# Kernel optimization log

Hardware: AMD Instinct MI355X
Metric: run time of the kernel (lower is better)

The kernel has to match this reference:

```python
import jax, jax.numpy as jnp
import numpy as np

N = 4096
D_IN = 512
D_OUT = 512

def setup_inputs() -> dict:
    key = jax.random.key(0)
    k1, k2, k3 = jax.random.split(key, 3)
    X = jax.random.normal(k1, (N, D_IN), dtype=jnp.float32)
    A = jax.random.uniform(k2, (N, N), dtype=jnp.float32)
    # Linear(input_dim, output_dim, bias=False): W is [out, in], y = x @ W.T
    W = jax.random.normal(k3, (D_OUT, D_IN), dtype=jnp.float32) * (1.0 / np.sqrt(D_IN))
    return {"X": X, "A": A, "W": W}

def reference(X, A, W):
    # A2 = A + I
    A2 = A + jnp.eye(A.shape[0], dtype=A.dtype)
    # Dhat = diag(diagonal(A2)); fractional_matrix_power(Dhat, -1/2) on a
    # diagonal matrix is elementwise d^{-1/2}; dense diag GEMMs reduce to
    # row/column scaling.
    dscale = jnp.diagonal(A2) ** (-0.5)  # [N]
    temp = (A2 @ X) @ W.T                # [N, D_OUT]
    A_norm = dscale[:, None] * A2 * dscale[None, :]  # D^-1/2 A2 D^-1/2
    return jax.nn.relu(A_norm @ temp)
```

## Files before the change

### kernel.cpp

```cpp
#include <hip/hip_runtime.h>
#include <hip/hip_bf16.h>
#include <stdint.h>

typedef float  f32x4  __attribute__((ext_vector_type(4)));
typedef __bf16 bf16x8 __attribute__((ext_vector_type(8)));
typedef unsigned short us4 __attribute__((ext_vector_type(4)));

#define NDIM 4096
#define DDIM 512
#define PSTRIDE 2097152

__device__ __forceinline__ unsigned short f2bf(float f) {
    union { float f; uint32_t u; } v; v.f = f;
    uint32_t u = v.u;
    u += 0x7FFFu + ((u >> 16) & 1u);
    return (unsigned short)(u >> 16);
}

__global__ void prep_kernel(const float* __restrict__ A, const float* __restrict__ X,
                            const float* __restrict__ W,
                            unsigned short* __restrict__ A2, unsigned short* __restrict__ Xb,
                            unsigned short* __restrict__ Wb, float* __restrict__ ds) {
    const int b = blockIdx.x, tid = threadIdx.x;
    if (b < 16384) {
        int i = b * 256 + tid;
        int e = i << 2;
        int row = e >> 12, col = e & 4095;
        f32x4 v = ((const f32x4*)A)[i];
        int d = row - col;
        if (d >= 0 && d < 4) v[d] += 1.0f;
        us4 o; o.x = f2bf(v.x); o.y = f2bf(v.y); o.z = f2bf(v.z); o.w = f2bf(v.w);
        ((us4*)A2)[i] = o;
    } else if (b < 18432) {
        int i = (b - 16384) * 256 + tid;
        f32x4 v = ((const f32x4*)X)[i];
        us4 o; o.x = f2bf(v.x); o.y = f2bf(v.y); o.z = f2bf(v.z); o.w = f2bf(v.w);
        ((us4*)Xb)[i] = o;
    } else if (b < 18688) {
        int i = (b - 18432) * 256 + tid;
        f32x4 v = ((const f32x4*)W)[i];
        us4 o; o.x = f2bf(v.x); o.y = f2bf(v.y); o.z = f2bf(v.z); o.w = f2bf(v.w);
        ((us4*)Wb)[i] = o;
    } else {
        int i = (b - 18688) * 256 + tid;
        if (i < NDIM) ds[i] = rsqrtf(A[(size_t)i * (NDIM + 1)] + 1.0f);
    }
}

template <int MODE, int SWAP>
__global__ __launch_bounds__(256, 4) void gemm_bt(
    const unsigned short* __restrict__ A,
    const unsigned short* __restrict__ B,
    void* __restrict__ C,
    int K, int kc, int ldc)
{
    __shared__ unsigned short lsA[128 * 64];
    __shared__ unsigned short lsB[128 * 64];

    const int tid  = threadIdx.x;
    const int wid  = tid >> 6;
    const int lane = tid & 63;
    const int m0 = (SWAP ? blockIdx.y : blockIdx.x) * 128;
    const int n0 = (SWAP ? blockIdx.x : blockIdx.y) * 128;
    const int kbase = blockIdx.z * kc;
    const int wm = (wid & 1) * 64;
    const int wn = (wid >> 1) * 64;

    const int lrow = lane >> 3;
    const int lcs  = (lane & 7) * 16;

    f32x4 acc[4][4];
    #pragma unroll
    for (int i = 0; i < 4; i++)
        #pragma unroll
        for (int j = 0; j < 4; j++) acc[i][j] = (f32x4)0.0f;

    const char* gA = (const char*)A + ((size_t)(m0 + wid * 32 + lrow) * K) * 2 + lcs;
    const char* gB = (const char*)B + ((size_t)(n0 + wid * 32 + lrow) * K) * 2 + lcs;
    const size_t rowstep = (size_t)8 * K * 2;

    for (int k0 = kbase; k0 < kbase + kc; k0 += 64) {
        const size_t kb = (size_t)k0 * 2;
        #pragma unroll
        for (int i = 0; i < 4; i++) {
            __builtin_amdgcn_global_load_lds(
                (const __attribute__((address_space(1))) void*)(gA + kb + (size_t)i * rowstep),
                (__attribute__((address_space(3))) void*)(&lsA[(wid * 4 + i) * 512]),
                16, 0, 0);
            __builtin_amdgcn_global_load_lds(
                (const __attribute__((address_space(1))) void*)(gB + kb + (size_t)i * rowstep),
                (__attribute__((address_space(3))) void*)(&lsB[(wid * 4 + i) * 512]),
                16, 0, 0);
        }
        __syncthreads();

        #pragma unroll
        for (int ks = 0; ks < 2; ks++) {
            const int kboff = ks * 64 + (lane >> 4) * 16;
            bf16x8 bfrag[4], afrag[4];
            #pragma unroll
            for (int nt = 0; nt < 4; nt++) {
                int r = wn + nt * 16 + (lane & 15);
                bfrag[nt] = *(const bf16x8*)((const char*)lsB + r * 128 + kboff);
            }
            #pragma unroll
            for (int mt = 0; mt < 4; mt++) {
                int r = wm + mt * 16 + (lane & 15);
                afrag[mt] = *(const bf16x8*)((const char*)lsA + r * 128 + kboff);
            }
            #pragma unroll
            for (int mt = 0; mt < 4; mt++)
                #pragma unroll
                for (int nt = 0; nt < 4; nt++)
                    acc[mt][nt] = __builtin_amdgcn_mfma_f32_16x16x32_bf16(
                        afrag[mt], bfrag[nt], acc[mt][nt], 0, 0, 0);
        }
        __syncthreads();
    }

    const int col  = lane & 15;
    const int quad = lane >> 4;
    #pragma unroll
    for (int mt = 0; mt < 4; mt++) {
        const int gm0 = m0 + wm + mt * 16 + quad * 4;
        #pragma unroll
        for (int nt = 0; nt < 4; nt++) {
            const int gn = n0 + wn + nt * 16 + col;
            f32x4 v = acc[mt][nt];
            if (MODE == 0) {
                us4 o;
                o.x = f2bf(v.x); o.y = f2bf(v.y); o.z = f2bf(v.z); o.w = f2bf(v.w);
                *(us4*)((unsigned short*)C + (size_t)gn * ldc + gm0) = o;
            } else {
                float* o = (float*)C + (size_t)blockIdx.z * PSTRIDE + (size_t)gm0 * ldc + gn;
                o[0]               = v.x;
                o[ldc]             = v.y;
                o[2 * (size_t)ldc] = v.z;
                o[3 * (size_t)ldc] = v.w;
            }
        }
    }
}

__global__ void ep2_kernel(const float* __restrict__ P, const float* __restrict__ ds,
                           unsigned short* __restrict__ T2) {
    int t = blockIdx.x * 256 + threadIdx.x;
    int e = t << 2;
    int i = e & 4095;
    f32x4 v = ((const f32x4*)P)[t];
    v += ((const f32x4*)(P + PSTRIDE))[t];
    v += ((const f32x4*)(P + 2 * PSTRIDE))[t];
    v += ((const f32x4*)(P + 3 * PSTRIDE))[t];
    f32x4 d = *(const f32x4*)(ds + i);
    us4 o;
    o.x = f2bf(v.x * d.x); o.y = f2bf(v.y * d.y);
    o.z = f2bf(v.z * d.z); o.w = f2bf(v.w * d.w);
    ((us4*)T2)[t] = o;
}

__global__ void ep3_kernel(const float* __restrict__ Q, const float* __restrict__ ds,
                           float* __restrict__ out) {
    int t = blockIdx.x * 256 + threadIdx.x;
    int e = t << 2;
    int i = e >> 9;
    float s = ds[i];
    f32x4 v = ((const f32x4*)Q)[t];
    v += ((const f32x4*)(Q + PSTRIDE))[t];
    v += ((const f32x4*)(Q + 2 * PSTRIDE))[t];
    v += ((const f32x4*)(Q + 3 * PSTRIDE))[t];
    f32x4 o;
    o.x = fmaxf(v.x * s, 0.0f); o.y = fmaxf(v.y * s, 0.0f);
    o.z = fmaxf(v.z * s, 0.0f); o.w = fmaxf(v.w * s, 0.0f);
    ((f32x4*)out)[t] = o;
}

extern "C" void kernel_launch(void* const* d_in, const int* in_sizes, int n_in,
                              void* d_out, int out_size, void* d_ws, size_t ws_size,
                              hipStream_t stream) {
    const float* X = (const float*)d_in[0];
    const float* A = (const float*)d_in[1];
    const float* W = (const float*)d_in[2];

    char* ws = (char*)d_ws;
    float*          dsc  = (float*)ws;
    unsigned short* A2   = (unsigned short*)(ws + 16384);
    unsigned short* Xb   = (unsigned short*)(ws + 33570816u);
    unsigned short* Wb   = (unsigned short*)(ws + 37765120u);
    unsigned short* Yt   = (unsigned short*)(ws + 38289408u);
    unsigned short* T2   = (unsigned short*)(ws + 42483712u);
    float*          Part = (float*)(ws + 46678016u);

    prep_kernel<<<18704, 256, 0, stream>>>(A, X, W, A2, Xb, Wb, dsc);

    gemm_bt<0, 0><<<dim3(32, 4, 1), 256, 0, stream>>>(Xb, Wb, Yt, 512, 512, 4096);
    gemm_bt<2, 1><<<dim3(32, 4, 4), 256, 0, stream>>>(Yt, A2, Part, 4096, 1024, 4096);
    ep2_kernel<<<2048, 256, 0, stream>>>(Part, dsc, T2);
    gemm_bt<2, 0><<<dim3(32, 4, 4), 256, 0, stream>>>(A2, T2, Part, 4096, 1024, 512);
    ep3_kernel<<<2048, 256, 0, stream>>>(Part, dsc, (float*)d_out);
}
```

Baseline: 191.6 us.

## Load small GEMM operand directly to registers, deepen K tile to 128

```diff
diff --git a/kernel.cpp b/kernel.cpp
--- a/kernel.cpp
+++ b/kernel.cpp
@@ -47,15 +47,20 @@
     }
 }
 
-template <int MODE, int SWAP>
-__global__ __launch_bounds__(256, 4) void gemm_bt(
+template <int MODE, int SWAP, int BK, int DIRA, int DIRB>
+__global__ __launch_bounds__(256, 2) void gemm_bt(
     const unsigned short* __restrict__ A,
     const unsigned short* __restrict__ B,
     void* __restrict__ C,
     int K, int kc, int ldc)
 {
-    __shared__ unsigned short lsA[128 * 64];
-    __shared__ unsigned short lsB[128 * 64];
+    constexpr int LPR = BK / 8;
+    constexpr int RPI = 64 / LPR;
+    constexpr int IPW = 128 / (4 * RPI);
+    constexpr int KS  = BK / 32;
+
+    __shared__ unsigned short lsA[DIRA ? 64 : 128 * BK];
+    __shared__ unsigned short lsB[DIRB ? 64 : 128 * BK];
 
     const int tid  = threadIdx.x;
     const int wid  = tid >> 6;
@@ -65,9 +70,11 @@
     const int kbase = blockIdx.z * kc;
     const int wm = (wid & 1) * 64;
     const int wn = (wid >> 1) * 64;
-
-    const int lrow = lane >> 3;
-    const int lcs  = (lane & 7) * 16;
+    const int quad = lane >> 4;
+    const int c16  = lane & 15;
+
+    const int lrow = lane / LPR;
+    const int lcs  = (lane % LPR) * 16;
 
     f32x4 acc[4][4];
     #pragma unroll
@@ -77,36 +84,70 @@
 
     const char* gA = (const char*)A + ((size_t)(m0 + wid * 32 + lrow) * K) * 2 + lcs;
     const char* gB = (const char*)B + ((size_t)(n0 + wid * 32 + lrow) * K) * 2 + lcs;
-    const size_t rowstep = (size_t)8 * K * 2;
-
-    for (int k0 = kbase; k0 < kbase + kc; k0 += 64) {
+    const size_t rowstep = (size_t)RPI * K * 2;
+
+    const char* aDir[4];
+    const char* bDir[4];
+    #pragma unroll
+    for (int t = 0; t < 4; t++) {
+        if (DIRA) aDir[t] = (const char*)A + ((size_t)(m0 + wm + t * 16 + c16) * K) * 2 + quad * 16;
+        if (DIRB) bDir[t] = (const char*)B + ((size_t)(n0 + wn + t * 16 + c16) * K) * 2 + quad * 16;
+    }
+
+    for (int k0 = kbase; k0 < kbase + kc; k0 += BK) {
         const size_t kb = (size_t)k0 * 2;
+        if (!DIRA) {
+            #pragma unroll
+            for (int i = 0; i < IPW; i++)
+                __builtin_amdgcn_global_load_lds(
+                    (const __attribute__((address_space(1))) void*)(gA + kb + (size_t)i * rowstep),
+                    (__attribute__((address_space(3))) void*)(&lsA[(wid * IPW + i) * 512]),
+                    16, 0, 0);
+        }
+        if (!DIRB) {
+            #pragma unroll
+            for (int i = 0; i < IPW; i++)
+                __builtin_amdgcn_global_load_lds(
+                    (const __attribute__((address_space(1))) void*)(gB + kb + (size_t)i * rowstep),
+                    (__attribute__((address_space(3))) void*)(&lsB[(wid * IPW + i) * 512]),
+                    16, 0, 0);
+        }
+        bf16x8 apre[KS][4], bpre[KS][4];
+        if (DIRA) {
+            #pragma unroll
+            for (int ks = 0; ks < KS; ks++)
+                #pragma unroll
+                for (int mt = 0; mt < 4; mt++)
+                    apre[ks][mt] = *(const bf16x8*)(aDir[mt] + kb + ks * 64);
+        }
+        if (DIRB) {
+            #pragma unroll
+            for (int ks = 0; ks < KS; ks++)
+                #pragma unroll
+                for (int nt = 0; nt < 4; nt++)
+                    bpre[ks][nt] = *(const bf16x8*)(bDir[nt] + kb + ks * 64);
+        }
+        __syncthreads();
+
         #pragma unroll
-        for (int i = 0; i < 4; i++) {
-            __builtin_amdgcn_global_load_lds(
-                (const __attribute__((address_space(1))) void*)(gA + kb + (size_t)i * rowstep),
-                (__attribute__((address_space(3))) void*)(&lsA[(wid * 4 + i) * 512]),
-                16, 0, 0);
-            __builtin_amdgcn_global_load_lds(
-                (const __attribute__((address_space(1))) void*)(gB + kb + (size_t)i * rowstep),
-                (__attribute__((address_space(3))) void*)(&lsB[(wid * 4 + i) * 512]),
-                16, 0, 0);
-        }
-        __syncthreads();
-
-        #pragma unroll
-        for (int ks = 0; ks < 2; ks++) {
-            const int kboff = ks * 64 + (lane >> 4) * 16;
+        for (int ks = 0; ks < KS; ks++) {
+            const int kboff = ks * 64 + quad * 16;
             bf16x8 bfrag[4], afrag[4];
             #pragma unroll
             for (int nt = 0; nt < 4; nt++) {
-                int r = wn + nt * 16 + (lane & 15);
-                bfrag[nt] = *(const bf16x8*)((const char*)lsB + r * 128 + kboff);
+                if (DIRB) bfrag[nt] = bpre[ks][nt];
+                else {
+                    int r = wn + nt * 16 + c16;
+                    bfrag[nt] = *(const bf16x8*)((const char*)lsB + r * (BK * 2) + kboff);
+                }
             }
             #pragma unroll
             for (int mt = 0; mt < 4; mt++) {
-                int r = wm + mt * 16 + (lane & 15);
-                afrag[mt] = *(const bf16x8*)((const char*)lsA + r * 128 + kboff);
+                if (DIRA) afrag[mt] = apre[ks][mt];
+                else {
+                    int r = wm + mt * 16 + c16;
+                    afrag[mt] = *(const bf16x8*)((const char*)lsA + r * (BK * 2) + kboff);
+                }
             }
             #pragma unroll
             for (int mt = 0; mt < 4; mt++)
@@ -118,14 +159,12 @@
         __syncthreads();
     }
 
-    const int col  = lane & 15;
-    const int quad = lane >> 4;
     #pragma unroll
     for (int mt = 0; mt < 4; mt++) {
         const int gm0 = m0 + wm + mt * 16 + quad * 4;
         #pragma unroll
         for (int nt = 0; nt < 4; nt++) {
-            const int gn = n0 + wn + nt * 16 + col;
+            const int gn = n0 + wn + nt * 16 + c16;
             f32x4 v = acc[mt][nt];
             if (MODE == 0) {
                 us4 o;
@@ -192,9 +231,9 @@
 
     prep_kernel<<<18704, 256, 0, stream>>>(A, X, W, A2, Xb, Wb, dsc);
 
-    gemm_bt<0, 0><<<dim3(32, 4, 1), 256, 0, stream>>>(Xb, Wb, Yt, 512, 512, 4096);
-    gemm_bt<2, 1><<<dim3(32, 4, 4), 256, 0, stream>>>(Yt, A2, Part, 4096, 1024, 4096);
+    gemm_bt<0, 0, 64, 0, 0><<<dim3(32, 4, 1), 256, 0, stream>>>(Xb, Wb, Yt, 512, 512, 4096);
+    gemm_bt<2, 1, 128, 1, 0><<<dim3(32, 4, 4), 256, 0, stream>>>(Yt, A2, Part, 4096, 1024, 4096);
     ep2_kernel<<<2048, 256, 0, stream>>>(Part, dsc, T2);
-    gemm_bt<2, 0><<<dim3(32, 4, 4), 256, 0, stream>>>(A2, T2, Part, 4096, 1024, 512);
+    gemm_bt<2, 0, 128, 0, 1><<<dim3(32, 4, 4), 256, 0, stream>>>(A2, T2, Part, 4096, 1024, 512);
     ep3_kernel<<<2048, 256, 0, stream>>>(Part, dsc, (float*)d_out);
 }
```

Result: slower. 228.1 us (+19.0%).
